# Kernel tuning notes

Hardware: AMD Instinct MI355X
Metric: run time of the kernel (lower is better)

## Reference

```python
import jax, jax.numpy as jnp
import numpy as np

N_DRUG = 10000
N_DIS = 10000
IN_UNITS = 256
N_EDGES = 1000000


def setup_inputs() -> dict:
    key = jax.random.key(0)
    ks = jax.random.split(key, 10)
    # Kaiming-uniform-ish init like torch Linear defaults
    def lin_w(k, fan_in, fan_out):
        bound = 1.0 / np.sqrt(fan_in)
        return jax.random.uniform(k, (fan_in, fan_out), jnp.float32, -bound, bound)
    return {
        "drug_feat": jax.random.normal(ks[0], (N_DRUG, IN_UNITS), jnp.float32),
        "dis_feat": jax.random.normal(ks[1], (N_DIS, IN_UNITS), jnp.float32),
        "src_idx": jax.random.randint(ks[2], (N_EDGES,), 0, N_DRUG, jnp.int64),
        "dst_idx": jax.random.randint(ks[3], (N_EDGES,), 0, N_DIS, jnp.int64),
        "W1": lin_w(ks[4], 2 * IN_UNITS, 128),
        "b1": jnp.zeros((128,), jnp.float32),
        "W2": lin_w(ks[5], 128, 64),
        "b2": jnp.zeros((64,), jnp.float32),
        "W3": lin_w(ks[6], 64, 1),
        "b3": jnp.zeros((1,), jnp.float32),
    }


def reference(drug_feat, dis_feat, src_idx, dst_idx, W1, b1, W2, b2, W3, b3):
    # apply_edges: gather src (drug) and dst (disease) features, concat -> [E, 2*in_units]
    m = jnp.concatenate([drug_feat[src_idx], dis_feat[dst_idx]], axis=1)
    # 3-layer MLP (dropout = identity in eval)
    h = jax.nn.relu(m @ W1 + b1)
    h = jax.nn.relu(h @ W2 + b2)
    out = h @ W3 + b3  # [E, 1]
    return out
```

## Files before the change

kernel.cpp:

```cpp
#include <hip/hip_runtime.h>
#include <hip/hip_bf16.h>

#define IN_UNITS 256
#define H1 128
#define H2 64

typedef __attribute__((ext_vector_type(8))) short bf16x8;
typedef __attribute__((ext_vector_type(4))) float f32x4;

union BV { uint4 u; __hip_bfloat162 h[4]; bf16x8 v; };

static __device__ __forceinline__ unsigned short bfbits(__hip_bfloat16 b) {
    union { __hip_bfloat16 b; unsigned short u; } c; c.b = b; return c.u;
}

__global__ __launch_bounds__(256) void pack_kernel(
    const float* __restrict__ W1, const float* __restrict__ W2,
    uint4* __restrict__ w1pack, uint4* __restrict__ w2pack)
{
    int b = blockIdx.x, t = threadIdx.x;
    if (b < 4) {
        int item = b * 256 + t;
        int f = item >> 6, l = item & 63;
        int ks = f >> 2, nt = f & 3;
        int row0 = ks * 32 + (l >> 4) * 8;
        int col  = nt * 16 + (l & 15);
        unsigned short h[8];
        #pragma unroll
        for (int j = 0; j < 8; ++j)
            h[j] = bfbits(__float2bfloat16(W2[(size_t)(row0 + j) * H2 + col]));
        uint4 v;
        v.x = (unsigned)h[0] | ((unsigned)h[1] << 16);
        v.y = (unsigned)h[2] | ((unsigned)h[3] << 16);
        v.z = (unsigned)h[4] | ((unsigned)h[5] << 16);
        v.w = (unsigned)h[6] | ((unsigned)h[7] << 16);
        w2pack[item] = v;
    } else {
        int idx = (b - 4) * 256 + t;
        int l = idx & 63, fr = idx >> 6;
        int hl = fr & 1, ntc = (fr >> 1) & 7, ks = (fr >> 4) & 7, side = fr >> 7;
        int row0 = side * IN_UNITS + ks * 32 + (l >> 4) * 8;
        int col  = ntc * 16 + (l & 15);
        unsigned short h[8];
        #pragma unroll
        for (int j = 0; j < 8; ++j) {
            float x = W1[(size_t)(row0 + j) * H1 + col];
            __hip_bfloat16 hi = __float2bfloat16(x);
            __hip_bfloat16 val = hi;
            if (hl) val = __float2bfloat16(x - __bfloat162float(hi));
            h[j] = bfbits(val);
        }
        uint4 v;
        v.x = (unsigned)h[0] | ((unsigned)h[1] << 16);
        v.y = (unsigned)h[2] | ((unsigned)h[3] << 16);
        v.z = (unsigned)h[4] | ((unsigned)h[5] << 16);
        v.w = (unsigned)h[6] | ((unsigned)h[7] << 16);
        w1pack[idx] = v;
    }
}

__global__ __launch_bounds__(256, 2) void proj_kernel(
    const float* __restrict__ drug_feat, const float* __restrict__ dis_feat,
    const uint4* __restrict__ w1pack, const float* __restrict__ b1,
    unsigned short* __restrict__ drug_bf, unsigned short* __restrict__ dis_bf,
    int n_rows)
{
    __shared__ uint4 w1s[4096];

    int t = threadIdx.x, lane = t & 63, wave = t >> 6;
    int b = blockIdx.x;
    int side = (b >> 1) & 1, ch = b & 1, group = b >> 2;

    #pragma unroll
    for (int i = 0; i < 16; ++i) {
        int li = i * 256 + t;
        int f_loc = li >> 6, l = li & 63;
        int f_glob = (side << 7) | ((f_loc >> 3) << 4) | (ch << 3) | (f_loc & 7);
        w1s[li] = w1pack[(size_t)f_glob * 64 + l];
    }
    __syncthreads();

    int mtile = group * 4 + wave;
    const float* feat = side ? dis_feat : drug_feat;
    unsigned short* outb = side ? dis_bf : drug_bf;
    int r0 = mtile * 16;
    int kb = (lane >> 4) * 8;
    int row = r0 + (lane & 15);
    if (row >= n_rows) row = n_rows - 1;

    f32x4 acc[4];
    #pragma unroll
    for (int nt = 0; nt < 4; ++nt) acc[nt] = (f32x4){0.f, 0.f, 0.f, 0.f};

    #pragma unroll
    for (int ks = 0; ks < 8; ++ks) {
        const float* ap = feat + (size_t)row * IN_UNITS + ks * 32 + kb;
        float4 x0 = *(const float4*)ap;
        float4 x1 = *(const float4*)(ap + 4);
        float xs[8] = {x0.x, x0.y, x0.z, x0.w, x1.x, x1.y, x1.z, x1.w};
        BV ahi, alo;
        #pragma unroll
        for (int p = 0; p < 4; ++p) {
            float2 pr = make_float2(xs[2 * p], xs[2 * p + 1]);
            __hip_bfloat162 hp = __float22bfloat162_rn(pr);
            ahi.h[p] = hp;
            float2 lo = make_float2(xs[2 * p]     - __bfloat162float(hp.x),
                                    xs[2 * p + 1] - __bfloat162float(hp.y));
            alo.h[p] = __float22bfloat162_rn(lo);
        }
        #pragma unroll
        for (int nt = 0; nt < 4; ++nt) {
            BV bhi, blo;
            bhi.u = w1s[(ks * 8 + nt * 2 + 0) * 64 + lane];
            blo.u = w1s[(ks * 8 + nt * 2 + 1) * 64 + lane];
            acc[nt] = __builtin_amdgcn_mfma_f32_16x16x32_bf16(ahi.v, bhi.v, acc[nt], 0, 0, 0);
            acc[nt] = __builtin_amdgcn_mfma_f32_16x16x32_bf16(alo.v, bhi.v, acc[nt], 0, 0, 0);
            acc[nt] = __builtin_amdgcn_mfma_f32_16x16x32_bf16(ahi.v, blo.v, acc[nt], 0, 0, 0);
        }
    }

    #pragma unroll
    for (int nt = 0; nt < 4; ++nt) {
        int col = ch * 64 + nt * 16 + (lane & 15);
        float bb = side ? b1[col] : 0.f;
        #pragma unroll
        for (int r = 0; r < 4; ++r) {
            int rr = r0 + (lane >> 4) * 4 + r;
            if (rr < n_rows)
                outb[(size_t)rr * H1 + col] = bfbits(__float2bfloat16(acc[nt][r] + bb));
        }
    }
}

__global__ __launch_bounds__(256, 3) void edge_kernel(
    const unsigned short* __restrict__ drug_bf, const unsigned short* __restrict__ dis_bf,
    const int* __restrict__ src_idx, const int* __restrict__ dst_idx,
    const uint4* __restrict__ w2pack, const float* __restrict__ b2,
    const float* __restrict__ W3, const float* __restrict__ b3,
    float* __restrict__ out, int n_edges)
{
    __shared__ uint4 w2s[1024];

    int t = threadIdx.x, lane = t & 63, wave = t >> 6;
    long e0 = ((long)blockIdx.x * 4 + wave) * 32;
    long emax = (long)n_edges - 1;

    long em0 = e0 + (lane & 15);       if (em0 > emax) em0 = emax;
    long em1 = e0 + 16 + (lane & 15);  if (em1 > emax) em1 = emax;
    int s0 = src_idx[em0], d0 = dst_idx[em0];
    int s1 = src_idx[em1], d1 = dst_idx[em1];

    int kb = (lane >> 4) * 8;
    const uint4* pa0 = (const uint4*)(drug_bf + (size_t)s0 * H1 + kb);
    const uint4* pc0 = (const uint4*)(dis_bf  + (size_t)d0 * H1 + kb);
    const uint4* pa1 = (const uint4*)(drug_bf + (size_t)s1 * H1 + kb);
    const uint4* pc1 = (const uint4*)(dis_bf  + (size_t)d1 * H1 + kb);
    uint4 ga0[4], gc0[4], ga1[4], gc1[4];
    #pragma unroll
    for (int ks = 0; ks < 4; ++ks) {
        ga0[ks] = pa0[ks * 4];
        gc0[ks] = pc0[ks * 4];
        ga1[ks] = pa1[ks * 4];
        gc1[ks] = pc1[ks * 4];
    }

    #pragma unroll
    for (int i = 0; i < 4; ++i) w2s[i * 256 + t] = w2pack[i * 256 + t];
    __syncthreads();

    float b2v[4], w3v[4];
    #pragma unroll
    for (int nt = 0; nt < 4; ++nt) {
        int col = (lane & 15) + nt * 16;
        b2v[nt] = b2[col];
        w3v[nt] = W3[col];
    }
    float b3v = b3[0];

    f32x4 acc[2][4];
    #pragma unroll
    for (int mt = 0; mt < 2; ++mt)
        #pragma unroll
        for (int nt = 0; nt < 4; ++nt)
            acc[mt][nt] = (f32x4){0.f, 0.f, 0.f, 0.f};

    __hip_bfloat162 z2 = __float22bfloat162_rn(make_float2(0.f, 0.f));

    #pragma unroll
    for (int ks = 0; ks < 4; ++ks) {
        BV a0, c0, a1, c1, r0v, r1v;
        a0.u = ga0[ks]; c0.u = gc0[ks];
        a1.u = ga1[ks]; c1.u = gc1[ks];
        #pragma unroll
        for (int j = 0; j < 4; ++j) {
            r0v.h[j] = __hmax2(__hadd2(a0.h[j], c0.h[j]), z2);
            r1v.h[j] = __hmax2(__hadd2(a1.h[j], c1.h[j]), z2);
        }
        #pragma unroll
        for (int nt = 0; nt < 4; ++nt) {
            BV bb; bb.u = w2s[(ks * 4 + nt) * 64 + lane];
            acc[0][nt] = __builtin_amdgcn_mfma_f32_16x16x32_bf16(r0v.v, bb.v, acc[0][nt], 0, 0, 0);
            acc[1][nt] = __builtin_amdgcn_mfma_f32_16x16x32_bf16(r1v.v, bb.v, acc[1][nt], 0, 0, 0);
        }
    }

    #pragma unroll
    for (int mt = 0; mt < 2; ++mt) {
        float part[4];
        #pragma unroll
        for (int r = 0; r < 4; ++r) {
            float p = 0.f;
            #pragma unroll
            for (int nt = 0; nt < 4; ++nt)
                p += fmaxf(acc[mt][nt][r] + b2v[nt], 0.f) * w3v[nt];
            part[r] = p;
        }
        #pragma unroll
        for (int off = 1; off <= 8; off <<= 1)
            #pragma unroll
            for (int r = 0; r < 4; ++r)
                part[r] += __shfl_xor(part[r], off, 64);
        if ((lane & 15) == 0) {
            #pragma unroll
            for (int r = 0; r < 4; ++r) {
                long e = e0 + mt * 16 + (lane >> 4) * 4 + r;
                if (e < n_edges) out[e] = part[r] + b3v;
            }
        }
    }
}

extern "C" void kernel_launch(void* const* d_in, const int* in_sizes, int n_in,
                              void* d_out, int out_size, void* d_ws, size_t ws_size,
                              hipStream_t stream) {
    const float* drug_feat = (const float*)d_in[0];
    const float* dis_feat  = (const float*)d_in[1];
    const int*   src_idx   = (const int*)d_in[2];
    const int*   dst_idx   = (const int*)d_in[3];
    const float* W1 = (const float*)d_in[4];
    const float* b1 = (const float*)d_in[5];
    const float* W2 = (const float*)d_in[6];
    const float* b2 = (const float*)d_in[7];
    const float* W3 = (const float*)d_in[8];
    const float* b3 = (const float*)d_in[9];
    float* out = (float*)d_out;

    int n_edges = in_sizes[2];
    int n_drug = in_sizes[0] / IN_UNITS;

    uint4* w2pack = (uint4*)d_ws;
    uint4* w1pack = (uint4*)((char*)d_ws + 16 * 1024);
    unsigned short* drug_bf = (unsigned short*)((char*)d_ws + (16 + 256) * 1024);
    unsigned short* dis_bf  = drug_bf + (size_t)n_drug * H1;

    pack_kernel<<<68, 256, 0, stream>>>(W1, W2, w1pack, w2pack);

    int groups = (((n_drug + 15) / 16) + 3) / 4;
    proj_kernel<<<groups * 4, 256, 0, stream>>>(
        drug_feat, dis_feat, w1pack, b1, drug_bf, dis_bf, n_drug);

    int edge_blocks = (n_edges + 127) / 128;
    edge_kernel<<<edge_blocks, 256, 0, stream>>>(
        drug_bf, dis_bf, src_idx, dst_idx, w2pack, b2, W3, b3, out, n_edges);
}
```

Measured before the change: 166.6 us.

## Switch to fp16 MFMA, drop split-precision W1 and LDS staging in projection

```diff
diff --git a/kernel.cpp b/kernel.cpp
--- a/kernel.cpp
+++ b/kernel.cpp
@@ -1,18 +1,21 @@
 #include <hip/hip_runtime.h>
-#include <hip/hip_bf16.h>
+#include <hip/hip_fp16.h>
 
 #define IN_UNITS 256
 #define H1 128
 #define H2 64
 
-typedef __attribute__((ext_vector_type(8))) short bf16x8;
-typedef __attribute__((ext_vector_type(4))) float f32x4;
-
-union BV { uint4 u; __hip_bfloat162 h[4]; bf16x8 v; };
-
-static __device__ __forceinline__ unsigned short bfbits(__hip_bfloat16 b) {
-    union { __hip_bfloat16 b; unsigned short u; } c; c.b = b; return c.u;
-}
+typedef _Float16 f16x8 __attribute__((ext_vector_type(8)));
+typedef _Float16 f16x2 __attribute__((ext_vector_type(2)));
+typedef float f32x4 __attribute__((ext_vector_type(4)));
+
+union HV { uint4 u; f16x8 v; };
+
+static __device__ __forceinline__ unsigned short h2bits(_Float16 x) {
+    union { _Float16 h; unsigned short u; } c; c.h = x; return c.u;
+}
+
+#define KEEP4(q) asm volatile("" : "+v"(q.x), "+v"(q.y), "+v"(q.z), "+v"(q.w))
 
 __global__ __launch_bounds__(256) void pack_kernel(
     const float* __restrict__ W1, const float* __restrict__ W2,
@@ -28,7 +31,7 @@
         unsigned short h[8];
         #pragma unroll
         for (int j = 0; j < 8; ++j)
-            h[j] = bfbits(__float2bfloat16(W2[(size_t)(row0 + j) * H2 + col]));
+            h[j] = h2bits((_Float16)W2[(size_t)(row0 + j) * H2 + col]);
         uint4 v;
         v.x = (unsigned)h[0] | ((unsigned)h[1] << 16);
         v.y = (unsigned)h[2] | ((unsigned)h[3] << 16);
@@ -37,19 +40,14 @@
         w2pack[item] = v;
     } else {
         int idx = (b - 4) * 256 + t;
-        int l = idx & 63, fr = idx >> 6;
-        int hl = fr & 1, ntc = (fr >> 1) & 7, ks = (fr >> 4) & 7, side = fr >> 7;
+        int l = idx & 63, f = idx >> 6;
+        int nt = f & 3, ch = (f >> 2) & 1, ks = (f >> 3) & 7, side = f >> 6;
         int row0 = side * IN_UNITS + ks * 32 + (l >> 4) * 8;
-        int col  = ntc * 16 + (l & 15);
+        int col  = ch * 64 + nt * 16 + (l & 15);
         unsigned short h[8];
         #pragma unroll
-        for (int j = 0; j < 8; ++j) {
-            float x = W1[(size_t)(row0 + j) * H1 + col];
-            __hip_bfloat16 hi = __float2bfloat16(x);
-            __hip_bfloat16 val = hi;
-            if (hl) val = __float2bfloat16(x - __bfloat162float(hi));
-            h[j] = bfbits(val);
-        }
+        for (int j = 0; j < 8; ++j)
+            h[j] = h2bits((_Float16)W1[(size_t)(row0 + j) * H1 + col]);
         uint4 v;
         v.x = (unsigned)h[0] | ((unsigned)h[1] << 16);
         v.y = (unsigned)h[2] | ((unsigned)h[3] << 16);
@@ -59,63 +57,45 @@
     }
 }
 
-__global__ __launch_bounds__(256, 2) void proj_kernel(
+__global__ __launch_bounds__(256) __attribute__((amdgpu_waves_per_eu(2, 2)))
+void proj_kernel(
     const float* __restrict__ drug_feat, const float* __restrict__ dis_feat,
     const uint4* __restrict__ w1pack, const float* __restrict__ b1,
-    unsigned short* __restrict__ drug_bf, unsigned short* __restrict__ dis_bf,
+    unsigned short* __restrict__ drug_h, unsigned short* __restrict__ dis_h,
     int n_rows)
 {
-    __shared__ uint4 w1s[4096];
-
     int t = threadIdx.x, lane = t & 63, wave = t >> 6;
-    int b = blockIdx.x;
-    int side = (b >> 1) & 1, ch = b & 1, group = b >> 2;
-
-    #pragma unroll
-    for (int i = 0; i < 16; ++i) {
-        int li = i * 256 + t;
-        int f_loc = li >> 6, l = li & 63;
-        int f_glob = (side << 7) | ((f_loc >> 3) << 4) | (ch << 3) | (f_loc & 7);
-        w1s[li] = w1pack[(size_t)f_glob * 64 + l];
-    }
-    __syncthreads();
-
-    int mtile = group * 4 + wave;
+    int side = wave >> 1, ch = wave & 1;
+    int mtile = blockIdx.x;
     const float* feat = side ? dis_feat : drug_feat;
-    unsigned short* outb = side ? dis_bf : drug_bf;
-    int r0 = mtile * 16;
+    unsigned short* outb = side ? dis_h : drug_h;
+
+    int row = mtile * 16 + (lane & 15);
+    if (row >= n_rows) row = n_rows - 1;
     int kb = (lane >> 4) * 8;
-    int row = r0 + (lane & 15);
-    if (row >= n_rows) row = n_rows - 1;
-
+
+    float4 fx[16];
+    #pragma unroll
+    for (int i = 0; i < 16; ++i)
+        fx[i] = *(const float4*)(feat + (size_t)row * IN_UNITS + (i >> 1) * 32 + kb + (i & 1) * 4);
+
+    int fbase = side * 64 + ch * 4;
     f32x4 acc[4];
     #pragma unroll
     for (int nt = 0; nt < 4; ++nt) acc[nt] = (f32x4){0.f, 0.f, 0.f, 0.f};
 
     #pragma unroll
     for (int ks = 0; ks < 8; ++ks) {
-        const float* ap = feat + (size_t)row * IN_UNITS + ks * 32 + kb;
-        float4 x0 = *(const float4*)ap;
-        float4 x1 = *(const float4*)(ap + 4);
-        float xs[8] = {x0.x, x0.y, x0.z, x0.w, x1.x, x1.y, x1.z, x1.w};
-        BV ahi, alo;
-        #pragma unroll
-        for (int p = 0; p < 4; ++p) {
-            float2 pr = make_float2(xs[2 * p], xs[2 * p + 1]);
-            __hip_bfloat162 hp = __float22bfloat162_rn(pr);
-            ahi.h[p] = hp;
-            float2 lo = make_float2(xs[2 * p]     - __bfloat162float(hp.x),
-                                    xs[2 * p + 1] - __bfloat162float(hp.y));
-            alo.h[p] = __float22bfloat162_rn(lo);
-        }
+        float4 x0 = fx[ks * 2], x1 = fx[ks * 2 + 1];
+        f16x8 a;
+        a[0] = (_Float16)x0.x; a[1] = (_Float16)x0.y;
+        a[2] = (_Float16)x0.z; a[3] = (_Float16)x0.w;
+        a[4] = (_Float16)x1.x; a[5] = (_Float16)x1.y;
+        a[6] = (_Float16)x1.z; a[7] = (_Float16)x1.w;
         #pragma unroll
         for (int nt = 0; nt < 4; ++nt) {
-            BV bhi, blo;
-            bhi.u = w1s[(ks * 8 + nt * 2 + 0) * 64 + lane];
-            blo.u = w1s[(ks * 8 + nt * 2 + 1) * 64 + lane];
-            acc[nt] = __builtin_amdgcn_mfma_f32_16x16x32_bf16(ahi.v, bhi.v, acc[nt], 0, 0, 0);
-            acc[nt] = __builtin_amdgcn_mfma_f32_16x16x32_bf16(alo.v, bhi.v, acc[nt], 0, 0, 0);
-            acc[nt] = __builtin_amdgcn_mfma_f32_16x16x32_bf16(ahi.v, blo.v, acc[nt], 0, 0, 0);
+            HV bb; bb.u = w1pack[(size_t)(fbase + ks * 8 + nt) * 64 + lane];
+            acc[nt] = __builtin_amdgcn_mfma_f32_16x16x32_f16(a, bb.v, acc[nt], 0, 0, 0);
         }
     }
 
@@ -125,15 +105,16 @@
         float bb = side ? b1[col] : 0.f;
         #pragma unroll
         for (int r = 0; r < 4; ++r) {
-            int rr = r0 + (lane >> 4) * 4 + r;
+            int rr = mtile * 16 + (lane >> 4) * 4 + r;
             if (rr < n_rows)
-                outb[(size_t)rr * H1 + col] = bfbits(__float2bfloat16(acc[nt][r] + bb));
-        }
-    }
-}
-
-__global__ __launch_bounds__(256, 3) void edge_kernel(
-    const unsigned short* __restrict__ drug_bf, const unsigned short* __restrict__ dis_bf,
+                outb[(size_t)rr * H1 + col] = h2bits((_Float16)(acc[nt][r] + bb));
+        }
+    }
+}
+
+__global__ __launch_bounds__(256) __attribute__((amdgpu_waves_per_eu(3, 3)))
+void edge_kernel(
+    const unsigned short* __restrict__ drug_h, const unsigned short* __restrict__ dis_h,
     const int* __restrict__ src_idx, const int* __restrict__ dst_idx,
     const uint4* __restrict__ w2pack, const float* __restrict__ b2,
     const float* __restrict__ W3, const float* __restrict__ b3,
@@ -142,19 +123,19 @@
     __shared__ uint4 w2s[1024];
 
     int t = threadIdx.x, lane = t & 63, wave = t >> 6;
-    long e0 = ((long)blockIdx.x * 4 + wave) * 32;
-    long emax = (long)n_edges - 1;
-
-    long em0 = e0 + (lane & 15);       if (em0 > emax) em0 = emax;
-    long em1 = e0 + 16 + (lane & 15);  if (em1 > emax) em1 = emax;
-    int s0 = src_idx[em0], d0 = dst_idx[em0];
-    int s1 = src_idx[em1], d1 = dst_idx[em1];
+    int e0 = (blockIdx.x * 4 + wave) * 32;
+    int emax = n_edges - 1;
+
+    int i0 = e0 + (lane & 15);      if (i0 > emax) i0 = emax;
+    int i1 = e0 + 16 + (lane & 15); if (i1 > emax) i1 = emax;
+    int s0 = src_idx[i0], d0 = dst_idx[i0];
+    int s1 = src_idx[i1], d1 = dst_idx[i1];
 
     int kb = (lane >> 4) * 8;
-    const uint4* pa0 = (const uint4*)(drug_bf + (size_t)s0 * H1 + kb);
-    const uint4* pc0 = (const uint4*)(dis_bf  + (size_t)d0 * H1 + kb);
-    const uint4* pa1 = (const uint4*)(drug_bf + (size_t)s1 * H1 + kb);
-    const uint4* pc1 = (const uint4*)(dis_bf  + (size_t)d1 * H1 + kb);
+    const uint4* pa0 = (const uint4*)(drug_h + s0 * H1 + kb);
+    const uint4* pc0 = (const uint4*)(dis_h  + d0 * H1 + kb);
+    const uint4* pa1 = (const uint4*)(drug_h + s1 * H1 + kb);
+    const uint4* pc1 = (const uint4*)(dis_h  + d1 * H1 + kb);
     uint4 ga0[4], gc0[4], ga1[4], gc1[4];
     #pragma unroll
     for (int ks = 0; ks < 4; ++ks) {
@@ -164,10 +145,6 @@
         gc1[ks] = pc1[ks * 4];
     }
 
-    #pragma unroll
-    for (int i = 0; i < 4; ++i) w2s[i * 256 + t] = w2pack[i * 256 + t];
-    __syncthreads();
-
     float b2v[4], w3v[4];
     #pragma unroll
     for (int nt = 0; nt < 4; ++nt) {
@@ -177,6 +154,13 @@
     }
     float b3v = b3[0];
 
+    #pragma unroll
+    for (int i = 0; i < 4; ++i) w2s[i * 256 + t] = w2pack[i * 256 + t];
+
+    #pragma unroll
+    for (int ks = 0; ks < 4; ++ks) { KEEP4(ga0[ks]); KEEP4(gc0[ks]); KEEP4(ga1[ks]); KEEP4(gc1[ks]); }
+    __syncthreads();
+
     f32x4 acc[2][4];
     #pragma unroll
     for (int mt = 0; mt < 2; ++mt)
@@ -184,23 +168,19 @@
         for (int nt = 0; nt < 4; ++nt)
             acc[mt][nt] = (f32x4){0.f, 0.f, 0.f, 0.f};
 
-    __hip_bfloat162 z2 = __float22bfloat162_rn(make_float2(0.f, 0.f));
-
     #pragma unroll
     for (int ks = 0; ks < 4; ++ks) {
-        BV a0, c0, a1, c1, r0v, r1v;
+        HV a0, c0, a1, c1;
         a0.u = ga0[ks]; c0.u = gc0[ks];
         a1.u = ga1[ks]; c1.u = gc1[ks];
-        #pragma unroll
-        for (int j = 0; j < 4; ++j) {
-            r0v.h[j] = __hmax2(__hadd2(a0.h[j], c0.h[j]), z2);
-            r1v.h[j] = __hmax2(__hadd2(a1.h[j], c1.h[j]), z2);
-        }
+        f16x8 zero = (f16x8)(_Float16)0;
+        f16x8 r0v = __builtin_elementwise_max(a0.v + c0.v, zero);
+        f16x8 r1v = __builtin_elementwise_max(a1.v + c1.v, zero);
         #pragma unroll
         for (int nt = 0; nt < 4; ++nt) {
-            BV bb; bb.u = w2s[(ks * 4 + nt) * 64 + lane];
-            acc[0][nt] = __builtin_amdgcn_mfma_f32_16x16x32_bf16(r0v.v, bb.v, acc[0][nt], 0, 0, 0);
-            acc[1][nt] = __builtin_amdgcn_mfma_f32_16x16x32_bf16(r1v.v, bb.v, acc[1][nt], 0, 0, 0);
+            HV bb; bb.u = w2s[(ks * 4 + nt) * 64 + lane];
+            acc[0][nt] = __builtin_amdgcn_mfma_f32_16x16x32_f16(r0v, bb.v, acc[0][nt], 0, 0, 0);
+            acc[1][nt] = __builtin_amdgcn_mfma_f32_16x16x32_f16(r1v, bb.v, acc[1][nt], 0, 0, 0);
         }
     }
 
@@ -223,7 +203,7 @@
         if ((lane & 15) == 0) {
             #pragma unroll
             for (int r = 0; r < 4; ++r) {
-                long e = e0 + mt * 16 + (lane >> 4) * 4 + r;
+                int e = e0 + mt * 16 + (lane >> 4) * 4 + r;
                 if (e < n_edges) out[e] = part[r] + b3v;
             }
         }
@@ -249,17 +229,17 @@
     int n_drug = in_sizes[0] / IN_UNITS;
 
     uint4* w2pack = (uint4*)d_ws;
-    uint4* w1pack = (uint4*)((char*)d_ws + 16 * 1024);
-    unsigned short* drug_bf = (unsigned short*)((char*)d_ws + (16 + 256) * 1024);
-    unsigned short* dis_bf  = drug_bf + (size_t)n_drug * H1;
-
-    pack_kernel<<<68, 256, 0, stream>>>(W1, W2, w1pack, w2pack);
-
-    int groups = (((n_drug + 15) / 16) + 3) / 4;
-    proj_kernel<<<groups * 4, 256, 0, stream>>>(
-        drug_feat, dis_feat, w1pack, b1, drug_bf, dis_bf, n_drug);
+    uint4* w1pack = (uint4*)((char*)d_ws + 32 * 1024);
+    unsigned short* drug_h = (unsigned short*)((char*)d_ws + 192 * 1024);
+    unsigned short* dis_h  = drug_h + (size_t)n_drug * H1;
+
+    pack_kernel<<<36, 256, 0, stream>>>(W1, W2, w1pack, w2pack);
+
+    int mtiles = (n_drug + 15) / 16;
+    proj_kernel<<<mtiles, 256, 0, stream>>>(
+        drug_feat, dis_feat, w1pack, b1, drug_h, dis_h, n_drug);
 
     int edge_blocks = (n_edges + 127) / 128;
     edge_kernel<<<edge_blocks, 256, 0, stream>>>(
-        drug_bf, dis_bf, src_idx, dst_idx, w2pack, b2, W3, b3, out, n_edges);
-}
+        drug_h, dis_h, src_idx, dst_idx, w2pack, b2, W3, b3, out, n_edges);
+}
```

After: 170.9 us. +2.6%, slower.
